# Kernel optimization log

Hardware: AMD Instinct MI355X
Metric: run time of the kernel (lower is better)

## Reference

```python
import jax, jax.numpy as jnp
import numpy as np
import math

B, P, N, DM, H, DK, DH, DF = 2, 12, 170, 64, 8, 8, 32, 256
SQ = math.sqrt(DK)

def _ln(x, g, b):
    m = jnp.mean(x, -1, keepdims=True)
    v = jnp.var(x, -1, keepdims=True)
    return (x - m) / jnp.sqrt(v + 1e-5) * g + b

def _nozero_softmax(s):
    # faithful to nozero_softmax: mask = (s != 0), max over full row, +1e-5 in denom
    mask = (s != 0).astype(s.dtype)
    e = jnp.exp(s - jnp.max(s, -1, keepdims=True)) * mask
    return e / (jnp.sum(e, -1, keepdims=True) + 1e-5)

def _meta(c, w1, b1, w2, b2):
    # MetaLearner: [B,P,N,DM] -> [3,B,P,N,H,DK,DM]
    h = jax.nn.relu(c @ w1 + b1) @ w2 + b2
    h = h.reshape(c.shape[:3] + (3, H, DK, DM))
    return jnp.moveaxis(h, 3, 0)

def _mhlin(W, x):
    # multihead_linear_transform: per-position meta weight applied to x
    return jnp.einsum('bpnhkd,bpnd->bpnhk', W, x)

def _gdc(data, W1, W2):
    # Gated_Dynamic_Connection (noGC=False). data: [G,B,P,N,C]
    d = jnp.moveaxis(data, 0, 3)  # [B,P,N,G,C]
    a = jnp.einsum('bpngc,gcd->bpngd', d, W1)
    s = jax.nn.softmax(jax.nn.relu(jnp.einsum('bpngc,gcd->bpngd', d, W2)), axis=3)
    return jnp.sum(a * s, axis=3)  # [B,P,N,DM]

def _swish_gate(x, out, wg, bg, wo, bo):
    h = (x @ wg + bg) * out
    return (h * jax.nn.sigmoid(h)) @ wo + bo

def _spatial(Q, K, V, T):
    # adjacency-masked spatial attention. Dense-masked form is exactly the
    # scatter-into-zeros buffer of the original: zero where T==0, QK/sqrt(dk) on edges.
    s = jnp.einsum('bpihk,bpjhk->bphij', Q, K) / SQ
    Tb = T if T.ndim == 2 else T[:, :, None]  # adaptive graph [B,P,1,N,N]
    s = s * (Tb != 0)
    alpha = _nozero_softmax(s) * Tb
    return jnp.einsum('bphij,bpjhk->hbpik', alpha, V)  # [H,B,P,N,DK]

def _temporal(Q, K, V):
    s = jnp.einsum('bqnhk,bpnhk->bnhqp', Q, K) / SQ
    alpha = jax.nn.softmax(s, -1)
    return jnp.einsum('bnhqp,bpnhk->hbqnk', alpha, V)  # [H,B,P,N,DK]

def _retnet(Q, K, V, D):
    # multihead_temporal_regnet with g=1 leading dim folded in
    r = jnp.einsum('bqnhk,bpnhk->bnhqp', Q, K) / SQ
    r = r * D  # D: [H,P,P] causal decay
    rs = jnp.maximum(jnp.abs(jnp.sum(r, -1, keepdims=True)), 1.0)
    r = r / rs
    return jnp.einsum('bnhqp,bpnhk->hbqnk', r, V)  # [H,B,P,N,DK]

def _forward(x, c_x, enc, T, A, D, mr_w1, mr_b1, mr_w2, mr_b2, ms0_w1, ms0_b1, ms0_w2, ms0_b2, ms1_w1, ms1_b1, ms1_w2, ms1_b2, gr_W1, gr_W2, gs0_W1, gs0_W2, gs1_W1, gs1_W2, g2_W1, g2_W2, ge_W1, ge_W2, swr_wg, swr_bg, swr_wo, swr_bo, sws_wg, sws_bg, sws_wo, sws_bo, swe_wg, swe_bg, swe_wo, swe_bo, lnr_g, lnr_b, lns_g, lns_b, lne_g, lne_b, lnf_g, lnf_b, wq, wk, wv, f_w1, f_b1, f_w2, f_b2):
    # 1) RetNet-style temporal self retention (meta-learned QKV)
    W = _meta(c_x, mr_w1, mr_b1, mr_w2, mr_b2)
    o = _gdc(_retnet(_mhlin(W[0], x), _mhlin(W[1], x), _mhlin(W[2], x), D), gr_W1, gr_W2)
    o = _swish_gate(x, o, swr_wg, swr_bg, swr_wo, swr_bo)
    x1 = _ln(o + x, lnr_g, lnr_b)
    # 2) Spatial self attention: predefined graph + adaptive graph branches
    W0 = _meta(c_x, ms0_w1, ms0_b1, ms0_w2, ms0_b2)
    o0 = _gdc(_spatial(_mhlin(W0[0], x1), _mhlin(W0[1], x1), _mhlin(W0[2], x1), T), gs0_W1, gs0_W2)
    W1m = _meta(c_x, ms1_w1, ms1_b1, ms1_w2, ms1_b2)
    o1 = _gdc(_spatial(_mhlin(W1m[0], x1), _mhlin(W1m[1], x1), _mhlin(W1m[2], x1), A), gs1_W1, gs1_W2)
    o = _gdc(jnp.stack([o0, o1], 0), g2_W1, g2_W2)
    o = _swish_gate(x1, o, sws_wg, sws_bg, sws_wo, sws_bo)
    x2 = _ln(o + x1, lns_g, lns_b)
    # 3) Temporal encoder-decoder attention
    q = (x2 @ wq).reshape(B, P, N, H, DK)
    k = (enc @ wk).reshape(B, P, N, H, DK)
    v = (enc @ wv).reshape(B, P, N, H, DK)
    o = _gdc(_temporal(q, k, v), ge_W1, ge_W2)
    o = _swish_gate(x2, o, swe_wg, swe_bg, swe_wo, swe_bo)
    x3 = _ln(o + x2, lne_g, lne_b)
    # 4) FFN
    o = jax.nn.relu(x3 @ f_w1 + f_b1) @ f_w2 + f_b2
    return _ln(o + x3, lnf_g, lnf_b)


def setup_inputs() -> dict:
    key = jax.random.key(0)
    ks = iter(jax.random.split(key, 100))
    def rn(shape, s=0.05):
        return (jax.random.normal(next(ks), shape) * s).astype(jnp.float32)
    inp = {}
    inp['x'] = jax.random.normal(next(ks), (B, P, N, DM), jnp.float32)
    inp['c_x'] = jax.random.normal(next(ks), (B, P, N, DM), jnp.float32)
    inp['enc'] = jax.random.normal(next(ks), (B, P, N, DM), jnp.float32)
    mT = jax.random.uniform(next(ks), (N, N)) < 0.1
    inp['T'] = (jax.random.uniform(next(ks), (N, N)) * mT).astype(jnp.float32)
    mA = jax.random.uniform(next(ks), (B, P, N, N)) < 0.05
    inp['A'] = (jax.random.uniform(next(ks), (B, P, N, N)) * mA).astype(jnp.float32)
    q = np.arange(P)
    gam = 1.0 - 2.0 ** (-5.0 - np.arange(H))
    Dm = np.where(q[:, None] >= q[None, :], gam[:, None, None] ** (q[:, None] - q[None, :]), 0.0)
    inp['D'] = jnp.asarray(Dm, jnp.float32)  # [H,P,P]
    for p in ['mr', 'ms0', 'ms1']:
        inp[p + '_w1'] = rn((DM, DH)); inp[p + '_b1'] = jnp.zeros((DH,), jnp.float32)
        inp[p + '_w2'] = rn((DH, 3 * H * DK * DM)); inp[p + '_b2'] = jnp.zeros((3 * H * DK * DM,), jnp.float32)
    for p in ['gr', 'gs0', 'gs1', 'ge']:
        inp[p + '_W1'] = rn((H, DK, DM)); inp[p + '_W2'] = rn((H, DK, DM))
    inp['g2_W1'] = rn((2, DM, DM)); inp['g2_W2'] = rn((2, DM, DM))
    for p in ['swr', 'sws', 'swe']:
        inp[p + '_wg'] = rn((DM, DM)); inp[p + '_bg'] = jnp.zeros((DM,), jnp.float32)
        inp[p + '_wo'] = rn((DM, DM)); inp[p + '_bo'] = jnp.zeros((DM,), jnp.float32)
    for p in ['lnr', 'lns', 'lne', 'lnf']:
        inp[p + '_g'] = jnp.ones((DM,), jnp.float32); inp[p + '_b'] = jnp.zeros((DM,), jnp.float32)
    inp['wq'] = rn((DM, DM)); inp['wk'] = rn((DM, DM)); inp['wv'] = rn((DM, DM))
    inp['f_w1'] = rn((DM, DF)); inp['f_b1'] = jnp.zeros((DF,), jnp.float32)
    inp['f_w2'] = rn((DF, DM)); inp['f_b2'] = jnp.zeros((DM,), jnp.float32)
    return inp


def reference(x, c_x, enc, T, A, D, mr_w1, mr_b1, mr_w2, mr_b2, ms0_w1, ms0_b1, ms0_w2, ms0_b2, ms1_w1, ms1_b1, ms1_w2, ms1_b2, gr_W1, gr_W2, gs0_W1, gs0_W2, gs1_W1, gs1_W2, g2_W1, g2_W2, ge_W1, ge_W2, swr_wg, swr_bg, swr_wo, swr_bo, sws_wg, sws_bg, sws_wo, sws_bo, swe_wg, swe_bg, swe_wo, swe_bo, lnr_g, lnr_b, lns_g, lns_b, lne_g, lne_b, lnf_g, lnf_b, wq, wk, wv, f_w1, f_b1, f_w2, f_b2):
    return _forward(x, c_x, enc, T, A, D, mr_w1, mr_b1, mr_w2, mr_b2, ms0_w1, ms0_b1, ms0_w2, ms0_b2, ms1_w1, ms1_b1, ms1_w2, ms1_b2, gr_W1, gr_W2, gs0_W1, gs0_W2, gs1_W1, gs1_W2, g2_W1, g2_W2, ge_W1, ge_W2, swr_wg, swr_bg, swr_wo, swr_bo, sws_wg, sws_bg, sws_wo, sws_bo, swe_wg, swe_bg, swe_wo, swe_bo, lnr_g, lnr_b, lns_g, lns_b, lne_g, lne_b, lnf_g, lnf_b, wq, wk, wv, f_w1, f_b1, f_w2, f_b2)
```

## Files before the change

### kernel.cpp

```cpp
#include <hip/hip_runtime.h>
#include <hip/hip_bf16.h>
#include <math.h>

namespace {

constexpr int B_ = 2, P_ = 12, N_ = 170, DM_ = 64, H_ = 8, DK_ = 8, DH_ = 32, DF_ = 256;
constexpr int T_ = B_ * P_ * N_;
constexpr float SQRT_DK = 2.8284271247461903f;

constexpr int NG_ = 12;
constexpr int NC_ = 66;
constexpr int WFRAG_G = NG_ * NC_ * 64 * 8;

typedef __attribute__((ext_vector_type(4))) short short4v;
typedef __attribute__((ext_vector_type(8))) short short8v;
typedef __attribute__((ext_vector_type(4))) float float4v;

__device__ __forceinline__ unsigned short f2bf(float x) {
    union { float f; unsigned int u; } c; c.f = x;
    unsigned int r = (c.u + 0x7FFFu + ((c.u >> 16) & 1u)) >> 16;
    return (unsigned short)r;
}

__global__ void k_pre(const float* __restrict__ c_x,
                      const float* __restrict__ w1a, const float* __restrict__ b1a,
                      const float* __restrict__ w1b, const float* __restrict__ b1b,
                      const float* __restrict__ w1c, const float* __restrict__ b1c,
                      const float* __restrict__ w2a, const float* __restrict__ b2a,
                      const float* __restrict__ w2b, const float* __restrict__ b2b,
                      const float* __restrict__ w2c, const float* __restrict__ b2c,
                      float* __restrict__ hra, float* __restrict__ hrb,
                      float* __restrict__ hrc, unsigned short* __restrict__ Wfrag) {
    if (blockIdx.y == 0) {
        int idx = blockIdx.x * 256 + threadIdx.x;
        if (idx >= 3 * NG_ * NC_ * 64) return;
        int lane = idx & 63;
        int c = (idx >> 6) % NC_;
        int ng = (idx >> 6) / NC_ % NG_;
        int g = idx / (64 * NC_ * NG_);
        const float* w2 = g == 0 ? w2a : (g == 1 ? w2b : w2c);
        const float* b2 = g == 0 ? b2a : (g == 1 ? b2b : b2c);
        int m = ng * 16 + (lane & 15);
        int u = c >> 1;
        int d0 = (c & 1) * 32 + (lane >> 4) * 8;
        const float* src = (u < DH_) ? (w2 + u * 12288 + m * 64 + d0) : (b2 + m * 64 + d0);
        short8v o;
        #pragma unroll
        for (int j = 0; j < 8; ++j) o[j] = (short)f2bf(src[j]);
        *(short8v*)(Wfrag + (size_t)idx * 8) = o;
    } else {
        int z = blockIdx.y - 1;
        const float* w1 = z == 0 ? w1a : (z == 1 ? w1b : w1c);
        const float* b1 = z == 0 ? b1a : (z == 1 ? b1b : b1c);
        float* hr = z == 0 ? hra : (z == 1 ? hrb : hrc);
        int idx = blockIdx.x * 256 + threadIdx.x;
        if (idx >= T_ * DH_) return;
        int t = idx / DH_, j = idx % DH_;
        float acc = b1[j];
        const float* cx = c_x + t * DM_;
        #pragma unroll
        for (int d = 0; d < DM_; ++d) acc += cx[d] * w1[d * DH_ + j];
        hr[idx] = fmaxf(acc, 0.f);
    }
}

__global__ __launch_bounds__(256) void k_meta_gemm2(
    const float* __restrict__ hr0, const float* __restrict__ hr1,
    const float* __restrict__ xin,
    const unsigned short* __restrict__ Wf0, const unsigned short* __restrict__ Wf1,
    float* __restrict__ out0, float* __restrict__ out1) {
    const int bz = blockIdx.z;
    const float* hr = bz ? hr1 : hr0;
    const unsigned short* Wf = bz ? Wf1 : Wf0;
    float* out = bz ? out1 : out0;

    const int tid = threadIdx.x;
    const int wv = tid >> 6, lane = tid & 63;
    const int l15 = lane & 15, quad = lane >> 4;
    const int g16 = blockIdx.x * 4 + wv;
    if (g16 >= 255) return;
    const int t = g16 * 16 + l15;
    const int nb = blockIdx.y;

    const float* xp = xin + t * 64 + quad * 8;
    float4v xa = *(const float4v*)(xp);
    float4v xb = *(const float4v*)(xp + 4);
    float4v xc = *(const float4v*)(xp + 32);
    float4v xd = *(const float4v*)(xp + 36);
    float xr[16] = {xa.x, xa.y, xa.z, xa.w, xb.x, xb.y, xb.z, xb.w,
                    xc.x, xc.y, xc.z, xc.w, xd.x, xd.y, xd.z, xd.w};

    const float* hrp = hr + t * 32;
    float hrbuf[32];
    #pragma unroll
    for (int i = 0; i < 8; ++i) {
        float4v h4 = *(const float4v*)(hrp + i * 4);
        hrbuf[i * 4 + 0] = h4.x; hrbuf[i * 4 + 1] = h4.y;
        hrbuf[i * 4 + 2] = h4.z; hrbuf[i * 4 + 3] = h4.w;
    }

    float4v acc[4] = {{0.f,0.f,0.f,0.f},{0.f,0.f,0.f,0.f},
                      {0.f,0.f,0.f,0.f},{0.f,0.f,0.f,0.f}};

    const unsigned short* wb = Wf + ((size_t)(nb * 4) * NC_ * 64 + lane) * 8;
    const size_t qstride = (size_t)NC_ * 64 * 8;
    const size_t cstride = 64 * 8;

    short8v b[2][8];
    {
        const unsigned short* wc = wb;
        #pragma unroll
        for (int q = 0; q < 4; ++q) {
            b[0][2 * q]     = *(const short8v*)(wc + q * qstride);
            b[0][2 * q + 1] = *(const short8v*)(wc + q * qstride + cstride);
        }
    }
    #pragma unroll
    for (int u = 0; u < 33; ++u) {
        const int cur = u & 1, nxt = cur ^ 1;
        if (u + 1 < 33) {
            const unsigned short* wc = wb + (size_t)(2 * (u + 1)) * cstride;
            #pragma unroll
            for (int q = 0; q < 4; ++q) {
                b[nxt][2 * q]     = *(const short8v*)(wc + q * qstride);
                b[nxt][2 * q + 1] = *(const short8v*)(wc + q * qstride + cstride);
            }
        }
        float hrv = (u < 32) ? hrbuf[u] : 1.0f;
        short8v a0, a1;
        #pragma unroll
        for (int j = 0; j < 8; ++j) {
            a0[j] = (short)f2bf(hrv * xr[j]);
            a1[j] = (short)f2bf(hrv * xr[8 + j]);
        }
        #pragma unroll
        for (int q = 0; q < 4; ++q) {
            acc[q] = __builtin_amdgcn_mfma_f32_16x16x32_bf16(a0, b[cur][2 * q],     acc[q], 0, 0, 0);
            acc[q] = __builtin_amdgcn_mfma_f32_16x16x32_bf16(a1, b[cur][2 * q + 1], acc[q], 0, 0, 0);
        }
    }

    #pragma unroll
    for (int q = 0; q < 4; ++q) {
        #pragma unroll
        for (int r = 0; r < 4; ++r) {
            int tt = g16 * 16 + quad * 4 + r;
            out[tt * 192 + nb * 64 + q * 16 + l15] = acc[q][r];
        }
    }
}

__global__ __launch_bounds__(256) void k_retnet(const float* __restrict__ qkv,
                                                const float* __restrict__ Dm,
                                                float* __restrict__ att) {
    const int bn = blockIdx.x;
    const int b = bn / N_, n = bn % N_;
    __shared__ float S[12][192];
    __shared__ float Ds[8 * 145];
    const int tid = threadIdx.x;
    for (int e = tid; e < 12 * 192; e += 256) {
        int p = e / 192, c = e % 192;
        S[p][c] = qkv[((size_t)((b * P_ + p) * N_ + n)) * 192 + c];
    }
    for (int e = tid; e < 1152; e += 256) {
        Ds[(e / 144) * 145 + (e % 144)] = Dm[e];
    }
    __syncthreads();
    const int qq = tid >> 6;
    const int lane = tid & 63;
    const int h = lane >> 3, k = lane & 7;
    for (int q = qq; q < P_; q += 4) {
        float Qv = S[q][h * 8 + k];
        float r[P_];
        float rsum = 0.f;
        #pragma unroll
        for (int p = 0; p < P_; ++p) {
            float prod = Qv * S[p][64 + h * 8 + k];
            prod += __shfl_xor(prod, 1, 64);
            prod += __shfl_xor(prod, 2, 64);
            prod += __shfl_xor(prod, 4, 64);
            float s = (prod / SQRT_DK) * Ds[h * 145 + q * 12 + p];
            r[p] = s; rsum += s;
        }
        float rs = fmaxf(fabsf(rsum), 1.0f);
        float acc = 0.f;
        #pragma unroll
        for (int p = 0; p < P_; ++p) acc += (r[p] / rs) * S[p][128 + h * 8 + k];
        att[((size_t)((b * P_ + q) * N_ + n)) * 64 + lane] = acc;
    }
}

__global__ __launch_bounds__(256) void k_temporal(const float* __restrict__ qkv,
                                                  float* __restrict__ att) {
    const int bn = blockIdx.x;
    const int b = bn / N_, n = bn % N_;
    __shared__ float S[12][192];
    const int tid = threadIdx.x;
    for (int e = tid; e < 12 * 192; e += 256) {
        int p = e / 192, c = e % 192;
        S[p][c] = qkv[((size_t)((b * P_ + p) * N_ + n)) * 192 + c];
    }
    __syncthreads();
    const int qq = tid >> 6;
    const int lane = tid & 63;
    const int h = lane >> 3, k = lane & 7;
    for (int q = qq; q < P_; q += 4) {
        float Qv = S[q][h * 8 + k];
        float s[P_];
        float mx = -1e30f;
        #pragma unroll
        for (int p = 0; p < P_; ++p) {
            float prod = Qv * S[p][64 + h * 8 + k];
            prod += __shfl_xor(prod, 1, 64);
            prod += __shfl_xor(prod, 2, 64);
            prod += __shfl_xor(prod, 4, 64);
            float v = prod / SQRT_DK;
            s[p] = v; mx = fmaxf(mx, v);
        }
        float den = 0.f, acc = 0.f;
        #pragma unroll
        for (int p = 0; p < P_; ++p) {
            float e = expf(s[p] - mx);
            den += e;
            acc += e * S[p][128 + h * 8 + k];
        }
        att[((size_t)((b * P_ + q) * N_ + n)) * 64 + lane] = acc / den;
    }
}

__global__ __launch_bounds__(256) void k_spatial_sparse(
    const float* __restrict__ qkvA, const float* __restrict__ qkvB,
    const float* __restrict__ Tm, const float* __restrict__ Am,
    float* __restrict__ attA, float* __restrict__ attB) {
    const int bp = blockIdx.y;
    const int g = blockIdx.z;
    const float* qkv = g ? qkvB : qkvA;
    float* att = g ? attB : attA;

    __shared__ int2 elist[4][176];

    const int tid = threadIdx.x;
    const int wv = tid >> 6, lane = tid & 63;
    const int i = blockIdx.x * 4 + wv;
    if (i >= N_) return;

    int2* el = elist[wv];
    const float* Trow = g ? (Am + (size_t)(bp * N_ + i) * N_) : (Tm + (size_t)i * N_);
    int nnz = 0;
    #pragma unroll
    for (int c = 0; c < 3; ++c) {
        int j = c * 64 + lane;
        float w = (j < N_) ? Trow[j] : 0.f;
        unsigned long long m = __ballot(w != 0.f);
        if (w != 0.f) {
            int pos = nnz + (int)__popcll(m & ((1ull << lane) - 1ull));
            el[pos] = make_int2(j, __float_as_int(w));
        }
        nnz += (int)__popcll(m);
    }

    const float q = qkv[(size_t)(bp * N_ + i) * 192 + lane];
    float m = 0.f;
    float den = 0.f, acc = 0.f;
    int e = 0;
    for (; e + 1 < nnz; e += 2) {
        int2 e0 = el[e], e1 = el[e + 1];
        const float* r0 = qkv + (size_t)(bp * N_ + e0.x) * 192;
        const float* r1 = qkv + (size_t)(bp * N_ + e1.x) * 192;
        float k0 = r0[64 + lane], v0 = r0[128 + lane];
        float k1 = r1[64 + lane], v1 = r1[128 + lane];
        float p0 = q * k0, p1 = q * k1;
        p0 += __shfl_xor(p0, 1, 64); p1 += __shfl_xor(p1, 1, 64);
        p0 += __shfl_xor(p0, 2, 64); p1 += __shfl_xor(p1, 2, 64);
        p0 += __shfl_xor(p0, 4, 64); p1 += __shfl_xor(p1, 4, 64);
        float s0 = p0 / SQRT_DK, s1 = p1 / SQRT_DK;
        float mn = fmaxf(m, fmaxf(s0, s1));
        float cs = expf(m - mn);
        float x0 = (s0 != 0.f) ? expf(s0 - mn) : 0.f;
        float x1 = (s1 != 0.f) ? expf(s1 - mn) : 0.f;
        den = den * cs + x0 + x1;
        acc = acc * cs + x0 * __int_as_float(e0.y) * v0
                       + x1 * __int_as_float(e1.y) * v1;
        m = mn;
    }
    if (e < nnz) {
        int2 e0 = el[e];
        const float* r0 = qkv + (size_t)(bp * N_ + e0.x) * 192;
        float k0 = r0[64 + lane], v0 = r0[128 + lane];
        float p0 = q * k0;
        p0 += __shfl_xor(p0, 1, 64);
        p0 += __shfl_xor(p0, 2, 64);
        p0 += __shfl_xor(p0, 4, 64);
        float s0 = p0 / SQRT_DK;
        float mn = fmaxf(m, s0);
        float cs = expf(m - mn);
        float x0 = (s0 != 0.f) ? expf(s0 - mn) : 0.f;
        den = den * cs + x0;
        acc = acc * cs + x0 * __int_as_float(e0.y) * v0;
    }

    att[(size_t)(bp * N_ + i) * 64 + lane] = acc / (den + 1e-5f);
}

__device__ __forceinline__ float gdc8(const float* dv, const float* W1,
                                      const float* W2, int dm) {
    float a[8], s[8];
    #pragma unroll
    for (int g = 0; g < 8; ++g) {
        float aa = 0.f, ss = 0.f;
        #pragma unroll
        for (int c = 0; c < 8; ++c) {
            float d = dv[g * 8 + c];
            aa += d * W1[(g * 8 + c) * 64 + dm];
            ss += d * W2[(g * 8 + c) * 64 + dm];
        }
        a[g] = aa; s[g] = fmaxf(ss, 0.f);
    }
    float mx = s[0];
    #pragma unroll
    for (int g = 1; g < 8; ++g) mx = fmaxf(mx, s[g]);
    float den = 0.f, o = 0.f;
    #pragma unroll
    for (int g = 0; g < 8; ++g) { float e = expf(s[g] - mx); den += e; o += a[g] * e; }
    return o / den;
}

__device__ __forceinline__ float ln_out(float r, int dm, const float* g, const float* b) {
    float m = r, m2 = r * r;
    #pragma unroll
    for (int off = 32; off; off >>= 1) { m += __shfl_xor(m, off, 64); m2 += __shfl_xor(m2, off, 64); }
    m *= (1.f / 64.f); m2 *= (1.f / 64.f);
    float var = m2 - m * m;
    return (r - m) * rsqrtf(var + 1e-5f) * g[dm] + b[dm];
}

__global__ __launch_bounds__(64) void k_gsl(const float* __restrict__ att, const float* __restrict__ xin,
    const float* W1, const float* W2,
    const float* wg, const float* bg,
    const float* wo, const float* bo,
    const float* lng, const float* lnb, float* __restrict__ xout) {
    int t = blockIdx.x, dm = threadIdx.x;
    __shared__ float dv[64], xv[64], swv[64];
    dv[dm] = att[t * 64 + dm];
    xv[dm] = xin[t * 64 + dm];
    __syncthreads();
    float o = gdc8(dv, W1, W2, dm);
    float hg = bg[dm];
    #pragma unroll
    for (int d = 0; d < 64; ++d) hg += xv[d] * wg[d * 64 + dm];
    hg *= o;
    swv[dm] = hg / (1.f + expf(-hg));
    __syncthreads();
    float ov = bo[dm];
    #pragma unroll
    for (int d = 0; d < 64; ++d) ov += swv[d] * wo[d * 64 + dm];
    float r = ov + xv[dm];
    xout[t * 64 + dm] = ln_out(r, dm, lng, lnb);
}

__global__ __launch_bounds__(64) void k_spatial_fuse(
    const float* __restrict__ att0, const float* __restrict__ att1, const float* __restrict__ x1,
    const float* gs0_W1, const float* gs0_W2,
    const float* gs1_W1, const float* gs1_W2,
    const float* g2_W1, const float* g2_W2,
    const float* wg, const float* bg,
    const float* wo, const float* bo,
    const float* lng, const float* lnb, float* __restrict__ xout) {
    int t = blockIdx.x, dm = threadIdx.x;
    __shared__ float d0[64], d1[64], o0s[64], o1s[64], xv[64], swv[64];
    d0[dm] = att0[t * 64 + dm];
    d1[dm] = att1[t * 64 + dm];
    xv[dm] = x1[t * 64 + dm];
    __syncthreads();
    o0s[dm] = gdc8(d0, gs0_W1, gs0_W2, dm);
    o1s[dm] = gdc8(d1, gs1_W1, gs1_W2, dm);
    __syncthreads();
    float a0 = 0.f, s0 = 0.f, a1 = 0.f, s1 = 0.f;
    #pragma unroll
    for (int c = 0; c < 64; ++c) {
        a0 += o0s[c] * g2_W1[c * 64 + dm];
        s0 += o0s[c] * g2_W2[c * 64 + dm];
        a1 += o1s[c] * g2_W1[(64 + c) * 64 + dm];
        s1 += o1s[c] * g2_W2[(64 + c) * 64 + dm];
    }
    s0 = fmaxf(s0, 0.f); s1 = fmaxf(s1, 0.f);
    float mx = fmaxf(s0, s1);
    float e0 = expf(s0 - mx), e1 = expf(s1 - mx);
    float o = (a0 * e0 + a1 * e1) / (e0 + e1);
    float hg = bg[dm];
    #pragma unroll
    for (int d = 0; d < 64; ++d) hg += xv[d] * wg[d * 64 + dm];
    hg *= o;
    swv[dm] = hg / (1.f + expf(-hg));
    __syncthreads();
    float ov = bo[dm];
    #pragma unroll
    for (int d = 0; d < 64; ++d) ov += swv[d] * wo[d * 64 + dm];
    float r = ov + xv[dm];
    xout[t * 64 + dm] = ln_out(r, dm, lng, lnb);
}

__global__ __launch_bounds__(64) void k_qkvproj(const float* __restrict__ x2,
    const float* __restrict__ enc,
    const float* wq, const float* wk, const float* wv,
    float* __restrict__ qkv) {
    int t = blockIdx.x, dm = threadIdx.x;
    __shared__ float xv[64], ev[64];
    xv[dm] = x2[t * 64 + dm];
    ev[dm] = enc[t * 64 + dm];
    __syncthreads();
    float aq = 0.f, ak = 0.f, av = 0.f;
    #pragma unroll
    for (int d = 0; d < 64; ++d) {
        aq += xv[d] * wq[d * 64 + dm];
        ak += ev[d] * wk[d * 64 + dm];
        av += ev[d] * wv[d * 64 + dm];
    }
    qkv[t * 192 + dm] = aq;
    qkv[t * 192 + 64 + dm] = ak;
    qkv[t * 192 + 128 + dm] = av;
}

__global__ __launch_bounds__(64) void k_ffn(const float* __restrict__ x3,
    const float* w1, const float* b1,
    const float* w2, const float* b2,
    const float* lng, const float* lnb,
    float* __restrict__ out) {
    int t = blockIdx.x, dm = threadIdx.x;
    __shared__ float xv[64], hv[256];
    xv[dm] = x3[t * 64 + dm];
    __syncthreads();
    #pragma unroll
    for (int e = 0; e < 4; ++e) {
        int j = e * 64 + dm;
        float a = b1[j];
        #pragma unroll
        for (int d = 0; d < 64; ++d) a += xv[d] * w1[d * 256 + j];
        hv[j] = fmaxf(a, 0.f);
    }
    __syncthreads();
    float a = b2[dm];
    for (int j = 0; j < 256; ++j) a += hv[j] * w2[j * 64 + dm];
    float r = a + xv[dm];
    out[t * 64 + dm] = ln_out(r, dm, lng, lnb);
}

}

extern "C" void kernel_launch(void* const* d_in, const int* in_sizes, int n_in,
                              void* d_out, int out_size, void* d_ws, size_t ws_size,
                              hipStream_t stream) {
    (void)in_sizes; (void)n_in; (void)out_size; (void)ws_size;
    const float* x    = (const float*)d_in[0];
    const float* c_x  = (const float*)d_in[1];
    const float* enc  = (const float*)d_in[2];
    const float* Tm   = (const float*)d_in[3];
    const float* Am   = (const float*)d_in[4];
    const float* Dm   = (const float*)d_in[5];
    const float* mr_w1 = (const float*)d_in[6];
    const float* mr_b1 = (const float*)d_in[7];
    const float* mr_w2 = (const float*)d_in[8];
    const float* mr_b2 = (const float*)d_in[9];
    const float* ms0_w1 = (const float*)d_in[10];
    const float* ms0_b1 = (const float*)d_in[11];
    const float* ms0_w2 = (const float*)d_in[12];
    const float* ms0_b2 = (const float*)d_in[13];
    const float* ms1_w1 = (const float*)d_in[14];
    const float* ms1_b1 = (const float*)d_in[15];
    const float* ms1_w2 = (const float*)d_in[16];
    const float* ms1_b2 = (const float*)d_in[17];
    const float* gr_W1 = (const float*)d_in[18];
    const float* gr_W2 = (const float*)d_in[19];
    const float* gs0_W1 = (const float*)d_in[20];
    const float* gs0_W2 = (const float*)d_in[21];
    const float* gs1_W1 = (const float*)d_in[22];
    const float* gs1_W2 = (const float*)d_in[23];
    const float* g2_W1 = (const float*)d_in[24];
    const float* g2_W2 = (const float*)d_in[25];
    const float* ge_W1 = (const float*)d_in[26];
    const float* ge_W2 = (const float*)d_in[27];
    const float* swr_wg = (const float*)d_in[28];
    const float* swr_bg = (const float*)d_in[29];
    const float* swr_wo = (const float*)d_in[30];
    const float* swr_bo = (const float*)d_in[31];
    const float* sws_wg = (const float*)d_in[32];
    const float* sws_bg = (const float*)d_in[33];
    const float* sws_wo = (const float*)d_in[34];
    const float* sws_bo = (const float*)d_in[35];
    const float* swe_wg = (const float*)d_in[36];
    const float* swe_bg = (const float*)d_in[37];
    const float* swe_wo = (const float*)d_in[38];
    const float* swe_bo = (const float*)d_in[39];
    const float* lnr_g = (const float*)d_in[40];
    const float* lnr_b = (const float*)d_in[41];
    const float* lns_g = (const float*)d_in[42];
    const float* lns_b = (const float*)d_in[43];
    const float* lne_g = (const float*)d_in[44];
    const float* lne_b = (const float*)d_in[45];
    const float* lnf_g = (const float*)d_in[46];
    const float* lnf_b = (const float*)d_in[47];
    const float* wq = (const float*)d_in[48];
    const float* wk = (const float*)d_in[49];
    const float* wv = (const float*)d_in[50];
    const float* f_w1 = (const float*)d_in[51];
    const float* f_b1 = (const float*)d_in[52];
    const float* f_w2 = (const float*)d_in[53];
    const float* f_b2 = (const float*)d_in[54];

    float* ws   = (float*)d_ws;
    float* hr   = ws;
    float* hr2  = hr   + T_ * DH_;
    float* qkva = hr2  + T_ * DH_;
    float* qkvb = qkva + T_ * 192;
    float* atta = qkvb + T_ * 192;
    float* attb = atta + T_ * DM_;
    float* x1f  = attb + T_ * DM_;
    float* x2f  = x1f  + T_ * DM_;
    float* x3f  = x2f  + T_ * DM_;
    unsigned short* Wfrag = (unsigned short*)(x3f + T_ * DM_);
    float* hr_r = attb;

    k_pre<<<dim3(594, 4), 256, 0, stream>>>(
        c_x, mr_w1, mr_b1, ms0_w1, ms0_b1, ms1_w1, ms1_b1,
        mr_w2, mr_b2, ms0_w2, ms0_b2, ms1_w2, ms1_b2,
        hr_r, hr, hr2, Wfrag);

    k_meta_gemm2<<<dim3(64, 3, 1), 256, 0, stream>>>(
        hr_r, hr_r, x, Wfrag, Wfrag, qkva, qkva);
    k_retnet<<<B_ * N_, 256, 0, stream>>>(qkva, Dm, atta);
    k_gsl<<<T_, 64, 0, stream>>>(atta, x, gr_W1, gr_W2, swr_wg, swr_bg, swr_wo, swr_bo,
                                 lnr_g, lnr_b, x1f);

    k_meta_gemm2<<<dim3(64, 3, 2), 256, 0, stream>>>(
        hr, hr2, x1f, Wfrag + WFRAG_G, Wfrag + 2 * WFRAG_G, qkva, qkvb);
    k_spatial_sparse<<<dim3((N_ + 3) / 4, B_ * P_, 2), 256, 0, stream>>>(
        qkva, qkvb, Tm, Am, atta, attb);
    k_spatial_fuse<<<T_, 64, 0, stream>>>(atta, attb, x1f, gs0_W1, gs0_W2, gs1_W1, gs1_W2,
                                          g2_W1, g2_W2, sws_wg, sws_bg, sws_wo, sws_bo,
                                          lns_g, lns_b, x2f);

    k_qkvproj<<<T_, 64, 0, stream>>>(x2f, enc, wq, wk, wv, qkva);
    k_temporal<<<B_ * N_, 256, 0, stream>>>(qkva, atta);
    k_gsl<<<T_, 64, 0, stream>>>(atta, x2f, ge_W1, ge_W2, swe_wg, swe_bg, swe_wo, swe_bo,
                                 lne_g, lne_b, x3f);

    k_ffn<<<T_, 64, 0, stream>>>(x3f, f_w1, f_b1, f_w2, f_b2, lnf_g, lnf_b, (float*)d_out);
}
```

Baseline: 324.4 us.

## Stage per-token weight matrices in LDS and process eight tokens per block

```diff
diff --git a/kernel.cpp b/kernel.cpp
--- a/kernel.cpp
+++ b/kernel.cpp
@@ -20,6 +20,12 @@
     union { float f; unsigned int u; } c; c.f = x;
     unsigned int r = (c.u + 0x7FFFu + ((c.u >> 16) & 1u)) >> 16;
     return (unsigned short)r;
+}
+
+__device__ __forceinline__ void stage_w(float* dst, const float* __restrict__ src,
+                                        int nfloats, int tid) {
+    for (int e = tid * 4; e < nfloats; e += 1024)
+        *(float4v*)(dst + e) = *(const float4v*)(src + e);
 }
 
 __global__ void k_pre(const float* __restrict__ c_x,
@@ -334,115 +340,178 @@
     return (r - m) * rsqrtf(var + 1e-5f) * g[dm] + b[dm];
 }
 
-__global__ __launch_bounds__(64) void k_gsl(const float* __restrict__ att, const float* __restrict__ xin,
-    const float* W1, const float* W2,
-    const float* wg, const float* bg,
-    const float* wo, const float* bo,
-    const float* lng, const float* lnb, float* __restrict__ xout) {
-    int t = blockIdx.x, dm = threadIdx.x;
-    __shared__ float dv[64], xv[64], swv[64];
-    dv[dm] = att[t * 64 + dm];
-    xv[dm] = xin[t * 64 + dm];
-    __syncthreads();
-    float o = gdc8(dv, W1, W2, dm);
-    float hg = bg[dm];
-    #pragma unroll
-    for (int d = 0; d < 64; ++d) hg += xv[d] * wg[d * 64 + dm];
-    hg *= o;
-    swv[dm] = hg / (1.f + expf(-hg));
-    __syncthreads();
-    float ov = bo[dm];
-    #pragma unroll
-    for (int d = 0; d < 64; ++d) ov += swv[d] * wo[d * 64 + dm];
-    float r = ov + xv[dm];
-    xout[t * 64 + dm] = ln_out(r, dm, lng, lnb);
-}
-
-__global__ __launch_bounds__(64) void k_spatial_fuse(
-    const float* __restrict__ att0, const float* __restrict__ att1, const float* __restrict__ x1,
-    const float* gs0_W1, const float* gs0_W2,
-    const float* gs1_W1, const float* gs1_W2,
-    const float* g2_W1, const float* g2_W2,
-    const float* wg, const float* bg,
-    const float* wo, const float* bo,
-    const float* lng, const float* lnb, float* __restrict__ xout) {
-    int t = blockIdx.x, dm = threadIdx.x;
-    __shared__ float d0[64], d1[64], o0s[64], o1s[64], xv[64], swv[64];
-    d0[dm] = att0[t * 64 + dm];
-    d1[dm] = att1[t * 64 + dm];
-    xv[dm] = x1[t * 64 + dm];
-    __syncthreads();
-    o0s[dm] = gdc8(d0, gs0_W1, gs0_W2, dm);
-    o1s[dm] = gdc8(d1, gs1_W1, gs1_W2, dm);
-    __syncthreads();
-    float a0 = 0.f, s0 = 0.f, a1 = 0.f, s1 = 0.f;
-    #pragma unroll
-    for (int c = 0; c < 64; ++c) {
-        a0 += o0s[c] * g2_W1[c * 64 + dm];
-        s0 += o0s[c] * g2_W2[c * 64 + dm];
-        a1 += o1s[c] * g2_W1[(64 + c) * 64 + dm];
-        s1 += o1s[c] * g2_W2[(64 + c) * 64 + dm];
-    }
-    s0 = fmaxf(s0, 0.f); s1 = fmaxf(s1, 0.f);
-    float mx = fmaxf(s0, s1);
-    float e0 = expf(s0 - mx), e1 = expf(s1 - mx);
-    float o = (a0 * e0 + a1 * e1) / (e0 + e1);
-    float hg = bg[dm];
-    #pragma unroll
-    for (int d = 0; d < 64; ++d) hg += xv[d] * wg[d * 64 + dm];
-    hg *= o;
-    swv[dm] = hg / (1.f + expf(-hg));
-    __syncthreads();
-    float ov = bo[dm];
-    #pragma unroll
-    for (int d = 0; d < 64; ++d) ov += swv[d] * wo[d * 64 + dm];
-    float r = ov + xv[dm];
-    xout[t * 64 + dm] = ln_out(r, dm, lng, lnb);
-}
-
-__global__ __launch_bounds__(64) void k_qkvproj(const float* __restrict__ x2,
+__global__ __launch_bounds__(256) void k_gsl(const float* __restrict__ att,
+    const float* __restrict__ xin,
+    const float* __restrict__ W1, const float* __restrict__ W2,
+    const float* __restrict__ wg, const float* __restrict__ bg,
+    const float* __restrict__ wo, const float* __restrict__ bo,
+    const float* __restrict__ lng, const float* __restrict__ lnb,
+    float* __restrict__ xout) {
+    __shared__ float Wb[16384];
+    __shared__ float dvw[4][64], xvw[4][64], sww[4][64];
+    const int tid = threadIdx.x, wv = tid >> 6, lane = tid & 63;
+    stage_w(Wb,         W1, 4096, tid);
+    stage_w(Wb + 4096,  W2, 4096, tid);
+    stage_w(Wb + 8192,  wg, 4096, tid);
+    stage_w(Wb + 12288, wo, 4096, tid);
+    __syncthreads();
+    #pragma unroll
+    for (int s = 0; s < 2; ++s) {
+        const int t = blockIdx.x * 8 + wv * 2 + s;
+        dvw[wv][lane] = att[t * 64 + lane];
+        xvw[wv][lane] = xin[t * 64 + lane];
+        float o = gdc8(dvw[wv], Wb, Wb + 4096, lane);
+        float hg = bg[lane];
+        #pragma unroll
+        for (int d = 0; d < 64; ++d) hg += xvw[wv][d] * Wb[8192 + d * 64 + lane];
+        hg *= o;
+        sww[wv][lane] = hg / (1.f + expf(-hg));
+        float ov = bo[lane];
+        #pragma unroll
+        for (int d = 0; d < 64; ++d) ov += sww[wv][d] * Wb[12288 + d * 64 + lane];
+        float r = ov + xvw[wv][lane];
+        xout[t * 64 + lane] = ln_out(r, lane, lng, lnb);
+    }
+}
+
+__global__ __launch_bounds__(256) void k_spatial_fuse(
+    const float* __restrict__ att0, const float* __restrict__ att1,
+    const float* __restrict__ x1,
+    const float* __restrict__ gs0_W1, const float* __restrict__ gs0_W2,
+    const float* __restrict__ gs1_W1, const float* __restrict__ gs1_W2,
+    const float* __restrict__ g2_W1, const float* __restrict__ g2_W2,
+    const float* __restrict__ wg, const float* __restrict__ bg,
+    const float* __restrict__ wo, const float* __restrict__ bo,
+    const float* __restrict__ lng, const float* __restrict__ lnb,
+    float* __restrict__ x2f) {
+    __shared__ float Wb[16384];
+    __shared__ float o0s[8][64], o1s[8][64], xvs[8][64];
+    __shared__ float d0w[4][64], d1w[4][64], sww[4][64];
+    const int tid = threadIdx.x, wv = tid >> 6, lane = tid & 63;
+
+    stage_w(Wb,         gs0_W1, 4096, tid);
+    stage_w(Wb + 4096,  gs0_W2, 4096, tid);
+    stage_w(Wb + 8192,  gs1_W1, 4096, tid);
+    stage_w(Wb + 12288, gs1_W2, 4096, tid);
+    __syncthreads();
+    #pragma unroll
+    for (int s = 0; s < 2; ++s) {
+        const int t = blockIdx.x * 8 + wv * 2 + s, slot = wv * 2 + s;
+        d0w[wv][lane] = att0[t * 64 + lane];
+        d1w[wv][lane] = att1[t * 64 + lane];
+        xvs[slot][lane] = x1[t * 64 + lane];
+        o0s[slot][lane] = gdc8(d0w[wv], Wb, Wb + 4096, lane);
+        o1s[slot][lane] = gdc8(d1w[wv], Wb + 8192, Wb + 12288, lane);
+    }
+    __syncthreads();
+
+    stage_w(Wb,        g2_W1, 8192, tid);
+    stage_w(Wb + 8192, g2_W2, 8192, tid);
+    __syncthreads();
+    float oreg[2];
+    #pragma unroll
+    for (int s = 0; s < 2; ++s) {
+        const int slot = wv * 2 + s;
+        float a0 = 0.f, s0 = 0.f, a1 = 0.f, s1 = 0.f;
+        #pragma unroll
+        for (int c = 0; c < 64; ++c) {
+            float v0 = o0s[slot][c], v1 = o1s[slot][c];
+            a0 += v0 * Wb[c * 64 + lane];
+            s0 += v0 * Wb[8192 + c * 64 + lane];
+            a1 += v1 * Wb[(64 + c) * 64 + lane];
+            s1 += v1 * Wb[8192 + (64 + c) * 64 + lane];
+        }
+        s0 = fmaxf(s0, 0.f); s1 = fmaxf(s1, 0.f);
+        float mx = fmaxf(s0, s1);
+        float e0 = expf(s0 - mx), e1 = expf(s1 - mx);
+        oreg[s] = (a0 * e0 + a1 * e1) / (e0 + e1);
+    }
+    __syncthreads();
+
+    stage_w(Wb,        wg, 4096, tid);
+    stage_w(Wb + 4096, wo, 4096, tid);
+    __syncthreads();
+    #pragma unroll
+    for (int s = 0; s < 2; ++s) {
+        const int t = blockIdx.x * 8 + wv * 2 + s, slot = wv * 2 + s;
+        float hg = bg[lane];
+        #pragma unroll
+        for (int d = 0; d < 64; ++d) hg += xvs[slot][d] * Wb[d * 64 + lane];
+        hg *= oreg[s];
+        sww[wv][lane] = hg / (1.f + expf(-hg));
+        float ov = bo[lane];
+        #pragma unroll
+        for (int d = 0; d < 64; ++d) ov += sww[wv][d] * Wb[4096 + d * 64 + lane];
+        float r = ov + xvs[slot][lane];
+        x2f[t * 64 + lane] = ln_out(r, lane, lng, lnb);
+    }
+}
+
+__global__ __launch_bounds__(256) void k_qkvproj(const float* __restrict__ x2,
     const float* __restrict__ enc,
-    const float* wq, const float* wk, const float* wv,
+    const float* __restrict__ wq, const float* __restrict__ wk,
+    const float* __restrict__ wv,
     float* __restrict__ qkv) {
-    int t = blockIdx.x, dm = threadIdx.x;
-    __shared__ float xv[64], ev[64];
-    xv[dm] = x2[t * 64 + dm];
-    ev[dm] = enc[t * 64 + dm];
-    __syncthreads();
-    float aq = 0.f, ak = 0.f, av = 0.f;
-    #pragma unroll
-    for (int d = 0; d < 64; ++d) {
-        aq += xv[d] * wq[d * 64 + dm];
-        ak += ev[d] * wk[d * 64 + dm];
-        av += ev[d] * wv[d * 64 + dm];
-    }
-    qkv[t * 192 + dm] = aq;
-    qkv[t * 192 + 64 + dm] = ak;
-    qkv[t * 192 + 128 + dm] = av;
-}
-
-__global__ __launch_bounds__(64) void k_ffn(const float* __restrict__ x3,
-    const float* w1, const float* b1,
-    const float* w2, const float* b2,
-    const float* lng, const float* lnb,
+    __shared__ float Wb[12288];
+    __shared__ float xvw[4][64], evw[4][64];
+    const int tid = threadIdx.x, wvv = tid >> 6, lane = tid & 63;
+    stage_w(Wb,        wq, 4096, tid);
+    stage_w(Wb + 4096, wk, 4096, tid);
+    stage_w(Wb + 8192, wv, 4096, tid);
+    __syncthreads();
+    #pragma unroll
+    for (int s = 0; s < 2; ++s) {
+        const int t = blockIdx.x * 8 + wvv * 2 + s;
+        xvw[wvv][lane] = x2[t * 64 + lane];
+        evw[wvv][lane] = enc[t * 64 + lane];
+        float aq = 0.f, ak = 0.f, av = 0.f;
+        #pragma unroll
+        for (int d = 0; d < 64; ++d) {
+            aq += xvw[wvv][d] * Wb[d * 64 + lane];
+            ak += evw[wvv][d] * Wb[4096 + d * 64 + lane];
+            av += evw[wvv][d] * Wb[8192 + d * 64 + lane];
+        }
+        qkv[t * 192 + lane] = aq;
+        qkv[t * 192 + 64 + lane] = ak;
+        qkv[t * 192 + 128 + lane] = av;
+    }
+}
+
+__global__ __launch_bounds__(256) void k_ffn(const float* __restrict__ x3,
+    const float* __restrict__ w1, const float* __restrict__ b1,
+    const float* __restrict__ w2, const float* __restrict__ b2,
+    const float* __restrict__ lng, const float* __restrict__ lnb,
     float* __restrict__ out) {
-    int t = blockIdx.x, dm = threadIdx.x;
-    __shared__ float xv[64], hv[256];
-    xv[dm] = x3[t * 64 + dm];
-    __syncthreads();
-    #pragma unroll
-    for (int e = 0; e < 4; ++e) {
-        int j = e * 64 + dm;
-        float a = b1[j];
-        #pragma unroll
-        for (int d = 0; d < 64; ++d) a += xv[d] * w1[d * 256 + j];
-        hv[j] = fmaxf(a, 0.f);
-    }
-    __syncthreads();
-    float a = b2[dm];
-    for (int j = 0; j < 256; ++j) a += hv[j] * w2[j * 64 + dm];
-    float r = a + xv[dm];
-    out[t * 64 + dm] = ln_out(r, dm, lng, lnb);
+    __shared__ float Wb[16384];
+    __shared__ float hvs[8][256];
+    __shared__ float xvs[8][64];
+    const int tid = threadIdx.x, wv = tid >> 6, lane = tid & 63;
+    stage_w(Wb, w1, 16384, tid);
+    __syncthreads();
+    #pragma unroll
+    for (int s = 0; s < 2; ++s) {
+        const int t = blockIdx.x * 8 + wv * 2 + s, slot = wv * 2 + s;
+        xvs[slot][lane] = x3[t * 64 + lane];
+        #pragma unroll
+        for (int e = 0; e < 4; ++e) {
+            int j = e * 64 + lane;
+            float a = b1[j];
+            #pragma unroll
+            for (int d = 0; d < 64; ++d) a += xvs[slot][d] * Wb[d * 256 + j];
+            hvs[slot][j] = fmaxf(a, 0.f);
+        }
+    }
+    __syncthreads();
+    stage_w(Wb, w2, 16384, tid);
+    __syncthreads();
+    #pragma unroll
+    for (int s = 0; s < 2; ++s) {
+        const int t = blockIdx.x * 8 + wv * 2 + s, slot = wv * 2 + s;
+        float a = b2[lane];
+        for (int j = 0; j < 256; ++j) a += hvs[slot][j] * Wb[j * 64 + lane];
+        float r = a + xvs[slot][lane];
+        out[t * 64 + lane] = ln_out(r, lane, lng, lnb);
+    }
 }
 
 }
@@ -528,21 +597,22 @@
     k_meta_gemm2<<<dim3(64, 3, 1), 256, 0, stream>>>(
         hr_r, hr_r, x, Wfrag, Wfrag, qkva, qkva);
     k_retnet<<<B_ * N_, 256, 0, stream>>>(qkva, Dm, atta);
-    k_gsl<<<T_, 64, 0, stream>>>(atta, x, gr_W1, gr_W2, swr_wg, swr_bg, swr_wo, swr_bo,
-                                 lnr_g, lnr_b, x1f);
+    k_gsl<<<T_ / 8, 256, 0, stream>>>(atta, x, gr_W1, gr_W2, swr_wg, swr_bg,
+                                      swr_wo, swr_bo, lnr_g, lnr_b, x1f);
 
     k_meta_gemm2<<<dim3(64, 3, 2), 256, 0, stream>>>(
         hr, hr2, x1f, Wfrag + WFRAG_G, Wfrag + 2 * WFRAG_G, qkva, qkvb);
     k_spatial_sparse<<<dim3((N_ + 3) / 4, B_ * P_, 2), 256, 0, stream>>>(
         qkva, qkvb, Tm, Am, atta, attb);
-    k_spatial_fuse<<<T_, 64, 0, stream>>>(atta, attb, x1f, gs0_W1, gs0_W2, gs1_W1, gs1_W2,
-                                          g2_W1, g2_W2, sws_wg, sws_bg, sws_wo, sws_bo,
-                                          lns_g, lns_b, x2f);
-
-    k_qkvproj<<<T_, 64, 0, stream>>>(x2f, enc, wq, wk, wv, qkva);
+    k_spatial_fuse<<<T_ / 8, 256, 0, stream>>>(atta, attb, x1f,
+        gs0_W1, gs0_W2, gs1_W1, gs1_W2, g2_W1, g2_W2,
+        sws_wg, sws_bg, sws_wo, sws_bo, lns_g, lns_b, x2f);
+
+    k_qkvproj<<<T_ / 8, 256, 0, stream>>>(x2f, enc, wq, wk, wv, qkva);
     k_temporal<<<B_ * N_, 256, 0, stream>>>(qkva, atta);
-    k_gsl<<<T_, 64, 0, stream>>>(atta, x2f, ge_W1, ge_W2, swe_wg, swe_bg, swe_wo, swe_bo,
-                                 lne_g, lne_b, x3f);
-
-    k_ffn<<<T_, 64, 0, stream>>>(x3f, f_w1, f_b1, f_w2, f_b2, lnf_g, lnf_b, (float*)d_out);
-}
+    k_gsl<<<T_ / 8, 256, 0, stream>>>(atta, x2f, ge_W1, ge_W2, swe_wg, swe_bg,
+                                      swe_wo, swe_bo, lne_g, lne_b, x3f);
+
+    k_ffn<<<T_ / 8, 256, 0, stream>>>(x3f, f_w1, f_b1, f_w2, f_b2,
+                                      lnf_g, lnf_b, (float*)d_out);
+}
```

New measurement: 385.0 us. +18.7%, slower.
